# Kernel tuning notes

Hardware: AMD Instinct MI355X
Metric: run time of the kernel (lower is better)

Reference implementation:

```python
import jax, jax.numpy as jnp
import numpy as np

B, TQ, TK, D, H = 2, 2048, 2048, 1024, 16


def setup_inputs() -> dict:
    key = jax.random.key(0)
    ks = jax.random.split(key, 8)
    s = 1.0 / np.sqrt(D)
    x_q = jax.random.normal(ks[0], (B, TQ, D), jnp.float32)
    x_k = jax.random.normal(ks[1], (B, TK, D), jnp.float32)
    x_v = jax.random.normal(ks[2], (B, TK, D), jnp.float32)
    # causal mask, True = masked (matches masked_fill semantics)
    causal = jnp.triu(jnp.ones((TQ, TK), jnp.bool_), k=1)
    attn_mask = jnp.broadcast_to(causal, (B, TQ, TK))
    Wq = jax.random.normal(ks[3], (D, D), jnp.float32) * s
    Wk = jax.random.normal(ks[4], (D, D), jnp.float32) * s
    Wv = jax.random.normal(ks[5], (D, D), jnp.float32) * s
    Wo = jax.random.normal(ks[6], (D, D), jnp.float32) * s
    z = jnp.zeros((D,), jnp.float32)
    return {"x_q": x_q, "x_k": x_k, "x_v": x_v, "attn_mask": attn_mask,
            "Wq": Wq, "bq": z, "Wk": Wk, "bk": z, "Wv": Wv, "bv": z,
            "Wo": Wo, "bo": z, "n_heads": H}


def reference(x_q, x_k, x_v, attn_mask, Wq, bq, Wk, bk, Wv, bv, Wo, bo, n_heads):
    Bv, Tq, Dm = x_q.shape
    Tk = x_k.shape[1]
    dh = Dm // n_heads
    # nn.Linear: y = x @ W^T + b; split heads -> [B, H, T, dh]
    Q = (jnp.einsum('btd,od->bto', x_q, Wq) + bq).reshape(Bv, Tq, n_heads, dh).transpose(0, 2, 1, 3)
    K = (jnp.einsum('btd,od->bto', x_k, Wk) + bk).reshape(Bv, Tk, n_heads, dh).transpose(0, 2, 1, 3)
    V = (jnp.einsum('btd,od->bto', x_v, Wv) + bv).reshape(Bv, Tk, n_heads, dh).transpose(0, 2, 1, 3)
    scale = 1.0 / np.sqrt(dh).astype(np.float32)
    scores = jnp.einsum('bhqd,bhkd->bhqk', Q, K) * scale  # [B,H,Tq,Tk]
    scores = jnp.where(attn_mask[:, None, :, :], -jnp.inf, scores)
    A = jax.nn.softmax(scores, axis=-1)  # dropout p=0.0 -> identity
    out = jnp.einsum('bhqk,bhkd->bhqd', A, V)
    out = out.transpose(0, 2, 1, 3).reshape(Bv, Tq, Dm)
    return jnp.einsum('btd,od->bto', out, Wo) + bo
```

## Files before the change

### kernel.cpp

```cpp
#include <hip/hip_runtime.h>


typedef __attribute__((ext_vector_type(8))) __bf16 bf16x8;
typedef __attribute__((ext_vector_type(4))) float f32x4;
typedef unsigned short u16;

constexpr int BATCH  = 2;
constexpr int TSEQ   = 2048;
constexpr int DMODEL = 1024;
constexpr int NHEAD  = 16;
constexpr int DHEAD  = 64;
constexpr int MROWS  = BATCH * TSEQ;

static __device__ __forceinline__ u16 f2bf(float f) {
  union { float f; unsigned int u; } v; v.f = f;
  unsigned int u = v.u;
  return (u16)((u + 0x7fffu + ((u >> 16) & 1u)) >> 16);
}

static __device__ __forceinline__ void gload16(const void* g, void* l) {
  __builtin_amdgcn_global_load_lds(
      (const __attribute__((address_space(1))) void*)g,
      (__attribute__((address_space(3))) void*)l, 16, 0, 0);
}

__global__ __launch_bounds__(256) void cvt_multi(const float* __restrict__ s0,
                                                 const float* __restrict__ s1,
                                                 const float* __restrict__ s2,
                                                 const float* __restrict__ s3,
                                                 u16* __restrict__ d0, u16* __restrict__ d1,
                                                 u16* __restrict__ d2, u16* __restrict__ d3,
                                                 int n4) {
  const float* s; u16* d;
  switch (blockIdx.y) {
    case 0: s = s0; d = d0; break;
    case 1: s = s1; d = d1; break;
    case 2: s = s2; d = d2; break;
    default: s = s3; d = d3; break;
  }
  int i = blockIdx.x * 256 + threadIdx.x;
  if (i >= n4) return;
  float4 f = ((const float4*)s)[i];
  ushort4 o;
  o.x = f2bf(f.x); o.y = f2bf(f.y); o.z = f2bf(f.z); o.w = f2bf(f.w);
  ((ushort4*)d)[i] = o;
}

template <typename Epi>
static __device__ __forceinline__ void gemm_body(const u16* __restrict__ X_,
                                                 const u16* __restrict__ W_,
                                                 const float* __restrict__ bias,
                                                 Epi epi) {
  __shared__ __align__(16) u16 As[2][4096];
  __shared__ __align__(16) u16 Bs[2][4096];
  const int lane = threadIdx.x & 63, wave = threadIdx.x >> 6;
  const int l16 = lane & 15, lk = lane >> 4;
  const int wm = wave >> 2, wn = wave & 3;
  const int row0 = blockIdx.x * 128, col0 = blockIdx.y * 128;
  constexpr int K = DMODEL;
  const u16* ga = X_ + (size_t)(row0 + wave * 16 + l16) * K + lk * 8;
  const u16* gb = W_ + (size_t)(col0 + wave * 16 + l16) * K + lk * 8;
  f32x4 acc[4][2];
#pragma unroll
  for (int mt = 0; mt < 4; ++mt)
#pragma unroll
    for (int nt = 0; nt < 2; ++nt) acc[mt][nt] = (f32x4){0.f, 0.f, 0.f, 0.f};
  gload16(ga, &As[0][wave * 512]);
  gload16(gb, &Bs[0][wave * 512]);
  __syncthreads();
  int buf = 0;
  for (int ks = 0; ks < K / 32; ++ks) {
    if (ks + 1 < K / 32) {
      gload16(ga + (ks + 1) * 32, &As[buf ^ 1][wave * 512]);
      gload16(gb + (ks + 1) * 32, &Bs[buf ^ 1][wave * 512]);
    }
    bf16x8 a[4], b[2];
#pragma unroll
    for (int mt = 0; mt < 4; ++mt)
      a[mt] = *(const bf16x8*)&As[buf][(wm * 4 + mt) * 512 + lane * 8];
#pragma unroll
    for (int nt = 0; nt < 2; ++nt)
      b[nt] = *(const bf16x8*)&Bs[buf][(wn * 2 + nt) * 512 + lane * 8];
#pragma unroll
    for (int mt = 0; mt < 4; ++mt)
#pragma unroll
      for (int nt = 0; nt < 2; ++nt)
        acc[mt][nt] =
            __builtin_amdgcn_mfma_f32_16x16x32_bf16(a[mt], b[nt], acc[mt][nt], 0, 0, 0);
    __syncthreads();
    buf ^= 1;
  }
#pragma unroll
  for (int mt = 0; mt < 4; ++mt)
#pragma unroll
    for (int nt = 0; nt < 2; ++nt)
#pragma unroll
      for (int r = 0; r < 4; ++r) {
        int m = row0 + wm * 64 + mt * 16 + lk * 4 + r;
        int n = col0 + wn * 32 + nt * 16 + l16;
        float v = acc[mt][nt][r] + bias[n];
        epi(m, n, v);
      }
}

__global__ __launch_bounds__(512) void gemm_qkv(
    const u16* __restrict__ xq, const u16* __restrict__ xk, const u16* __restrict__ xv,
    const u16* __restrict__ wq, const u16* __restrict__ wk, const u16* __restrict__ wv,
    const float* __restrict__ bq, const float* __restrict__ bk, const float* __restrict__ bv,
    u16* __restrict__ Qh, u16* __restrict__ Kh, u16* __restrict__ Vt) {
  const int z = blockIdx.z;
  const u16* X = z == 0 ? xq : (z == 1 ? xk : xv);
  const u16* W = z == 0 ? wq : (z == 1 ? wk : wv);
  const float* bias = z == 0 ? bq : (z == 1 ? bk : bv);
  u16* O01 = z == 0 ? Qh : Kh;
  gemm_body(X, W, bias, [&](int m, int n, float v) {
    int bb = m >> 11, t = m & (TSEQ - 1);
    int h = n >> 6, dd = n & (DHEAD - 1);
    if (z == 0) v *= 0.125f;
    if (z == 2)
      Vt[(((size_t)(bb * NHEAD + h)) * DHEAD + dd) * TSEQ + t] = f2bf(v);
    else
      O01[(((size_t)(bb * NHEAD + h)) * TSEQ + t) * DHEAD + dd] = f2bf(v);
  });
}

__global__ __launch_bounds__(512) void gemm_o(const u16* __restrict__ AO,
                                              const u16* __restrict__ wo,
                                              const float* __restrict__ bias,
                                              float* __restrict__ out) {
  gemm_body(AO, wo, bias,
            [&](int m, int n, float v) { out[(size_t)m * DMODEL + n] = v; });
}

__global__ __launch_bounds__(512, 6) void flash_attn(const u16* __restrict__ Qh,
                                                     const u16* __restrict__ Kh,
                                                     const u16* __restrict__ Vt,
                                                     u16* __restrict__ AO) {
  const int lane = threadIdx.x & 63, wave = threadIdx.x >> 6;
  const int l16 = lane & 15, lk = lane >> 4;
  const int bh = blockIdx.x;
  const int qt = (gridDim.y - 1) - blockIdx.y;
  const int q0 = qt * 128;
  const int b = bh >> 4, h = bh & 15;

  __shared__ __align__(16) u16 Kl[2][4096];
  __shared__ __align__(16) u16 Vl[2][4096];
  __shared__ __align__(16) u16 plds[8][16][72];

  const u16* Qb = Qh + (size_t)bh * TSEQ * DHEAD;
  const u16* Kb = Kh + (size_t)bh * TSEQ * DHEAD;
  const u16* Vb = Vt + (size_t)bh * DHEAD * TSEQ;

  bf16x8 qf[2];
  {
    const u16* qp = Qb + (size_t)(q0 + wave * 16 + l16) * DHEAD + lk * 8;
    qf[0] = *(const bf16x8*)(qp);
    qf[1] = *(const bf16x8*)(qp + 32);
  }

  float mrow[4], lsum[4];
  f32x4 acco[4];
#pragma unroll
  for (int r = 0; r < 4; ++r) { mrow[r] = -1e30f; lsum[r] = 0.f; }
#pragma unroll
  for (int dt = 0; dt < 4; ++dt) acco[dt] = (f32x4){0.f, 0.f, 0.f, 0.f};

  auto stage_kv = [&](int bufi, int kbase) {
    int trow = (wave >> 1) * 16 + l16;
    int dhs = (wave & 1) * 4 + lk;
    gload16(Kb + (size_t)(kbase + trow) * DHEAD + dhs * 8, &Kl[bufi][wave * 512]);
    gload16(Vb + (size_t)trow * TSEQ + kbase + dhs * 8, &Vl[bufi][wave * 512]);
  };

  const int nkb = 2 * qt + 2;
  const int kbdiag = 2 * qt + (wave >> 2);
  stage_kv(0, 0);
  __syncthreads();
  int buf = 0;
  const int qrow_base = q0 + wave * 16 + 4 * lk;

  for (int kb = 0; kb < nkb; ++kb) {
    const int kbase = kb * 64;
    if (kb + 1 < nkb) stage_kv(buf ^ 1, kbase + 64);

    if (kb <= kbdiag) {
      f32x4 s[4];
#pragma unroll
      for (int nt = 0; nt < 4; ++nt) {
        bf16x8 k0f = *(const bf16x8*)&Kl[buf][nt * 1024 + lane * 8];
        bf16x8 k1f = *(const bf16x8*)&Kl[buf][nt * 1024 + 512 + lane * 8];
        f32x4 z = (f32x4){0.f, 0.f, 0.f, 0.f};
        z = __builtin_amdgcn_mfma_f32_16x16x32_bf16(qf[0], k0f, z, 0, 0, 0);
        z = __builtin_amdgcn_mfma_f32_16x16x32_bf16(qf[1], k1f, z, 0, 0, 0);
        s[nt] = z;
      }
      if (kb == kbdiag) {
#pragma unroll
        for (int nt = 0; nt < 4; ++nt)
#pragma unroll
          for (int r = 0; r < 4; ++r) {
            int kcol = kbase + nt * 16 + l16;
            s[nt][r] = (kcol <= qrow_base + r) ? s[nt][r] : -1e30f;
          }
      }
      float pmax[4];
      bool need = false;
#pragma unroll
      for (int r = 0; r < 4; ++r) {
        pmax[r] = fmaxf(fmaxf(s[0][r], s[1][r]), fmaxf(s[2][r], s[3][r]));
        need |= (pmax[r] > mrow[r] + 8.f);
      }
      if (__any(need)) {
#pragma unroll
        for (int r = 0; r < 4; ++r) {
          float mx = pmax[r];
#pragma unroll
          for (int off = 1; off < 16; off <<= 1) mx = fmaxf(mx, __shfl_xor(mx, off, 16));
          float mnew = fmaxf(mrow[r], mx);
          float alpha = __expf(mrow[r] - mnew);
          lsum[r] *= alpha;
#pragma unroll
          for (int dt = 0; dt < 4; ++dt) acco[dt][r] *= alpha;
          mrow[r] = mnew;
        }
      }
#pragma unroll
      for (int r = 0; r < 4; ++r)
#pragma unroll
        for (int nt = 0; nt < 4; ++nt) {
          float p = __expf(s[nt][r] - mrow[r]);
          s[nt][r] = p;
          lsum[r] += p;
        }
#pragma unroll
      for (int nt = 0; nt < 4; ++nt)
#pragma unroll
        for (int r = 0; r < 4; ++r)
          plds[wave][4 * lk + r][nt * 16 + l16] = f2bf(s[nt][r]);
      bf16x8 pf0 = *(const bf16x8*)&plds[wave][l16][lk * 8];
      bf16x8 pf1 = *(const bf16x8*)&plds[wave][l16][32 + lk * 8];
#pragma unroll
      for (int dt = 0; dt < 4; ++dt) {
        bf16x8 v0 = *(const bf16x8*)&Vl[buf][dt * 1024 + lane * 8];
        bf16x8 v1 = *(const bf16x8*)&Vl[buf][dt * 1024 + 512 + lane * 8];
        acco[dt] = __builtin_amdgcn_mfma_f32_16x16x32_bf16(pf0, v0, acco[dt], 0, 0, 0);
        acco[dt] = __builtin_amdgcn_mfma_f32_16x16x32_bf16(pf1, v1, acco[dt], 0, 0, 0);
      }
    }
    __syncthreads();
    buf ^= 1;
  }

#pragma unroll
  for (int r = 0; r < 4; ++r) {
    float t = lsum[r];
#pragma unroll
    for (int off = 1; off < 16; off <<= 1) t += __shfl_xor(t, off, 16);
    lsum[r] = 1.f / t;
  }
#pragma unroll
  for (int dt = 0; dt < 4; ++dt)
#pragma unroll
    for (int r = 0; r < 4; ++r) {
      int t = qrow_base + r;
      int col = h * DHEAD + dt * 16 + l16;
      AO[((size_t)(b * TSEQ + t)) * DMODEL + col] = f2bf(acco[dt][r] * lsum[r]);
    }
}

extern "C" void kernel_launch(void* const* d_in, const int* in_sizes, int n_in,
                              void* d_out, int out_size, void* d_ws, size_t ws_size,
                              hipStream_t stream) {
  const float* x_q = (const float*)d_in[0];
  const float* x_k = (const float*)d_in[1];
  const float* x_v = (const float*)d_in[2];
  const float* Wq = (const float*)d_in[4];
  const float* bq = (const float*)d_in[5];
  const float* Wk = (const float*)d_in[6];
  const float* bk = (const float*)d_in[7];
  const float* Wv = (const float*)d_in[8];
  const float* bv = (const float*)d_in[9];
  const float* Wo = (const float*)d_in[10];
  const float* bo = (const float*)d_in[11];

  const size_t nx = (size_t)MROWS * DMODEL;
  const size_t nw = (size_t)DMODEL * DMODEL;
  u16* ws   = (u16*)d_ws;
  u16* xq_b = ws;
  u16* xk_b = xq_b + nx;
  u16* xv_b = xk_b + nx;
  u16* wq_b = xv_b + nx;
  u16* wk_b = wq_b + nw;
  u16* wv_b = wk_b + nw;
  u16* wo_b = wv_b + nw;
  u16* Qh   = wo_b + nw;
  u16* Kh   = Qh + nx;
  u16* Vt   = Kh + nx;
  u16* AO   = Vt + nx;

  const int n4x = (int)(nx / 4), n4w = (int)(nw / 4);
  cvt_multi<<<dim3((n4x + 255) / 256, 3), 256, 0, stream>>>(
      x_q, x_k, x_v, nullptr, xq_b, xk_b, xv_b, nullptr, n4x);
  cvt_multi<<<dim3((n4w + 255) / 256, 4), 256, 0, stream>>>(
      Wq, Wk, Wv, Wo, wq_b, wk_b, wv_b, wo_b, n4w);

  gemm_qkv<<<dim3(MROWS / 128, DMODEL / 128, 3), 512, 0, stream>>>(
      xq_b, xk_b, xv_b, wq_b, wk_b, wv_b, bq, bk, bv, Qh, Kh, Vt);

  flash_attn<<<dim3(BATCH * NHEAD, TSEQ / 128), 512, 0, stream>>>(Qh, Kh, Vt, AO);

  gemm_o<<<dim3(MROWS / 128, DMODEL / 128), 512, 0, stream>>>(AO, wo_b, bo, (float*)d_out);
}
```

Before: 158.2 us.

## Retile projection GEMMs to 256-thread blocks and narrower output-GEMM tiles

The shared GEMM body is templated on the N tile width and now uses 4 waves of 256 threads instead of 8. Each wave computes a larger 64xBN/2 sub-tile and issues several LDS-staging loads per k-step. The output projection switches to 128x64 tiles, doubling its grid to 512 blocks so more CUs are filled. The intent is more MFMA work per wave and better occupancy (launch bounds 256,4), at the cost of more accumulator registers per thread and fewer waves to hide load latency.

```diff
diff --git a/kernel.cpp b/kernel.cpp
--- a/kernel.cpp
+++ b/kernel.cpp
@@ -46,45 +46,58 @@
   ((ushort4*)d)[i] = o;
 }
 
-template <typename Epi>
+template <int BN, typename Epi>
 static __device__ __forceinline__ void gemm_body(const u16* __restrict__ X_,
                                                  const u16* __restrict__ W_,
                                                  const float* __restrict__ bias,
                                                  Epi epi) {
-  __shared__ __align__(16) u16 As[2][4096];
-  __shared__ __align__(16) u16 Bs[2][4096];
+  constexpr int K = DMODEL;
+  constexpr int NT = BN / 32;
+  __shared__ __align__(16) u16 As[2][8 * 512];
+  __shared__ __align__(16) u16 Bs[2][(BN / 16) * 512];
   const int lane = threadIdx.x & 63, wave = threadIdx.x >> 6;
   const int l16 = lane & 15, lk = lane >> 4;
-  const int wm = wave >> 2, wn = wave & 3;
-  const int row0 = blockIdx.x * 128, col0 = blockIdx.y * 128;
-  constexpr int K = DMODEL;
-  const u16* ga = X_ + (size_t)(row0 + wave * 16 + l16) * K + lk * 8;
-  const u16* gb = W_ + (size_t)(col0 + wave * 16 + l16) * K + lk * 8;
-  f32x4 acc[4][2];
+  const int wm = wave >> 1, wn = wave & 1;
+  const int row0 = blockIdx.x * 128, col0 = blockIdx.y * BN;
+
+  const u16* ga = X_ + (size_t)(row0 + l16) * K + lk * 8;
+  const u16* gb = W_ + (size_t)(col0 + l16) * K + lk * 8;
+
+  f32x4 acc[4][NT];
 #pragma unroll
   for (int mt = 0; mt < 4; ++mt)
 #pragma unroll
-    for (int nt = 0; nt < 2; ++nt) acc[mt][nt] = (f32x4){0.f, 0.f, 0.f, 0.f};
-  gload16(ga, &As[0][wave * 512]);
-  gload16(gb, &Bs[0][wave * 512]);
+    for (int nt = 0; nt < NT; ++nt) acc[mt][nt] = (f32x4){0.f, 0.f, 0.f, 0.f};
+
+  auto stage = [&](int bufi, int ks) {
+#pragma unroll
+    for (int j = 0; j < 2; ++j) {
+      int s = j * 4 + wave;
+      gload16(ga + (size_t)s * 16 * K + ks * 32, &As[bufi][s * 512]);
+    }
+#pragma unroll
+    for (int j = 0; j < BN / 64; ++j) {
+      int s = j * 4 + wave;
+      gload16(gb + (size_t)s * 16 * K + ks * 32, &Bs[bufi][s * 512]);
+    }
+  };
+
+  stage(0, 0);
   __syncthreads();
   int buf = 0;
   for (int ks = 0; ks < K / 32; ++ks) {
-    if (ks + 1 < K / 32) {
-      gload16(ga + (ks + 1) * 32, &As[buf ^ 1][wave * 512]);
-      gload16(gb + (ks + 1) * 32, &Bs[buf ^ 1][wave * 512]);
-    }
-    bf16x8 a[4], b[2];
+    if (ks + 1 < K / 32) stage(buf ^ 1, ks + 1);
+    bf16x8 a[4], b[NT];
 #pragma unroll
     for (int mt = 0; mt < 4; ++mt)
       a[mt] = *(const bf16x8*)&As[buf][(wm * 4 + mt) * 512 + lane * 8];
 #pragma unroll
-    for (int nt = 0; nt < 2; ++nt)
-      b[nt] = *(const bf16x8*)&Bs[buf][(wn * 2 + nt) * 512 + lane * 8];
+    for (int nt = 0; nt < NT; ++nt)
+      b[nt] = *(const bf16x8*)&Bs[buf][(wn * NT + nt) * 512 + lane * 8];
 #pragma unroll
     for (int mt = 0; mt < 4; ++mt)
 #pragma unroll
-      for (int nt = 0; nt < 2; ++nt)
+      for (int nt = 0; nt < NT; ++nt)
         acc[mt][nt] =
             __builtin_amdgcn_mfma_f32_16x16x32_bf16(a[mt], b[nt], acc[mt][nt], 0, 0, 0);
     __syncthreads();
@@ -93,17 +106,17 @@
 #pragma unroll
   for (int mt = 0; mt < 4; ++mt)
 #pragma unroll
-    for (int nt = 0; nt < 2; ++nt)
+    for (int nt = 0; nt < NT; ++nt)
 #pragma unroll
       for (int r = 0; r < 4; ++r) {
         int m = row0 + wm * 64 + mt * 16 + lk * 4 + r;
-        int n = col0 + wn * 32 + nt * 16 + l16;
+        int n = col0 + wn * (BN / 2) + nt * 16 + l16;
         float v = acc[mt][nt][r] + bias[n];
         epi(m, n, v);
       }
 }
 
-__global__ __launch_bounds__(512) void gemm_qkv(
+__global__ __launch_bounds__(256, 4) void gemm_qkv(
     const u16* __restrict__ xq, const u16* __restrict__ xk, const u16* __restrict__ xv,
     const u16* __restrict__ wq, const u16* __restrict__ wk, const u16* __restrict__ wv,
     const float* __restrict__ bq, const float* __restrict__ bk, const float* __restrict__ bv,
@@ -113,7 +126,7 @@
   const u16* W = z == 0 ? wq : (z == 1 ? wk : wv);
   const float* bias = z == 0 ? bq : (z == 1 ? bk : bv);
   u16* O01 = z == 0 ? Qh : Kh;
-  gemm_body(X, W, bias, [&](int m, int n, float v) {
+  gemm_body<128>(X, W, bias, [&](int m, int n, float v) {
     int bb = m >> 11, t = m & (TSEQ - 1);
     int h = n >> 6, dd = n & (DHEAD - 1);
     if (z == 0) v *= 0.125f;
@@ -124,12 +137,12 @@
   });
 }
 
-__global__ __launch_bounds__(512) void gemm_o(const u16* __restrict__ AO,
-                                              const u16* __restrict__ wo,
-                                              const float* __restrict__ bias,
-                                              float* __restrict__ out) {
-  gemm_body(AO, wo, bias,
-            [&](int m, int n, float v) { out[(size_t)m * DMODEL + n] = v; });
+__global__ __launch_bounds__(256, 4) void gemm_o(const u16* __restrict__ AO,
+                                                 const u16* __restrict__ wo,
+                                                 const float* __restrict__ bias,
+                                                 float* __restrict__ out) {
+  gemm_body<64>(AO, wo, bias,
+                [&](int m, int n, float v) { out[(size_t)m * DMODEL + n] = v; });
 }
 
 __global__ __launch_bounds__(512, 6) void flash_attn(const u16* __restrict__ Qh,
@@ -304,10 +317,10 @@
   cvt_multi<<<dim3((n4w + 255) / 256, 4), 256, 0, stream>>>(
       Wq, Wk, Wv, Wo, wq_b, wk_b, wv_b, wo_b, n4w);
 
-  gemm_qkv<<<dim3(MROWS / 128, DMODEL / 128, 3), 512, 0, stream>>>(
+  gemm_qkv<<<dim3(MROWS / 128, DMODEL / 128, 3), 256, 0, stream>>>(
       xq_b, xk_b, xv_b, wq_b, wk_b, wv_b, bq, bk, bv, Qh, Kh, Vt);
 
   flash_attn<<<dim3(BATCH * NHEAD, TSEQ / 128), 512, 0, stream>>>(Qh, Kh, Vt, AO);
 
-  gemm_o<<<dim3(MROWS / 128, DMODEL / 128), 512, 0, stream>>>(AO, wo_b, bo, (float*)d_out);
-}
+  gemm_o<<<dim3(MROWS / 128, DMODEL / 64), 256, 0, stream>>>(AO, wo_b, bo, (float*)d_out);
+}
```

Measured after the change: 160.8 us. About the same (+1.6%).

## Deepen GEMM global-to-LDS pipeline to four buffers with explicit vmcnt waits

Applied to the files above, without the earlier changes.

Replaces the double-buffered K loop in the shared GEMM body with a four-stage ring that keeps three tiles in flight. Explicit s_waitcnt vmcnt counts and a single s_barrier per iteration replace the two __syncthreads calls, and MFMA issue is wrapped in raised wave priority. Launch bounds hint four blocks per CU. The aim is to hide global load latency in the QKV and output projections, at the cost of doubling GEMM LDS use, which may limit occupancy. It also relies on hand-counted vmcnt values being correct for buffer reuse safety.

```diff
diff --git a/kernel.cpp b/kernel.cpp
--- a/kernel.cpp
+++ b/kernel.cpp
@@ -51,29 +51,42 @@
                                                  const u16* __restrict__ W_,
                                                  const float* __restrict__ bias,
                                                  Epi epi) {
-  __shared__ __align__(16) u16 As[2][4096];
-  __shared__ __align__(16) u16 Bs[2][4096];
+  constexpr int K = DMODEL;
+  constexpr int NK = K / 32;
+  __shared__ __align__(16) u16 As[4][4096];
+  __shared__ __align__(16) u16 Bs[4][4096];
   const int lane = threadIdx.x & 63, wave = threadIdx.x >> 6;
   const int l16 = lane & 15, lk = lane >> 4;
   const int wm = wave >> 2, wn = wave & 3;
   const int row0 = blockIdx.x * 128, col0 = blockIdx.y * 128;
-  constexpr int K = DMODEL;
+
   const u16* ga = X_ + (size_t)(row0 + wave * 16 + l16) * K + lk * 8;
   const u16* gb = W_ + (size_t)(col0 + wave * 16 + l16) * K + lk * 8;
+
   f32x4 acc[4][2];
 #pragma unroll
   for (int mt = 0; mt < 4; ++mt)
 #pragma unroll
     for (int nt = 0; nt < 2; ++nt) acc[mt][nt] = (f32x4){0.f, 0.f, 0.f, 0.f};
-  gload16(ga, &As[0][wave * 512]);
-  gload16(gb, &Bs[0][wave * 512]);
-  __syncthreads();
-  int buf = 0;
-  for (int ks = 0; ks < K / 32; ++ks) {
-    if (ks + 1 < K / 32) {
-      gload16(ga + (ks + 1) * 32, &As[buf ^ 1][wave * 512]);
-      gload16(gb + (ks + 1) * 32, &Bs[buf ^ 1][wave * 512]);
-    }
+
+  auto stage = [&](int bufi, int ks) {
+    gload16(ga + ks * 32, &As[bufi][wave * 512]);
+    gload16(gb + ks * 32, &Bs[bufi][wave * 512]);
+  };
+
+  stage(0, 0);
+  stage(1, 1);
+  stage(2, 2);
+
+  for (int ks = 0; ks < NK; ++ks) {
+    const int buf = ks & 3;
+    if (ks < NK - 2)       asm volatile("s_waitcnt vmcnt(4)" ::: "memory");
+    else if (ks == NK - 2) asm volatile("s_waitcnt vmcnt(2)" ::: "memory");
+    else                   asm volatile("s_waitcnt vmcnt(0)" ::: "memory");
+    __builtin_amdgcn_s_barrier();
+    __builtin_amdgcn_sched_barrier(0);
+    if (ks + 3 < NK) stage((ks + 3) & 3, ks + 3);
+
     bf16x8 a[4], b[2];
 #pragma unroll
     for (int mt = 0; mt < 4; ++mt)
@@ -81,15 +94,16 @@
 #pragma unroll
     for (int nt = 0; nt < 2; ++nt)
       b[nt] = *(const bf16x8*)&Bs[buf][(wn * 2 + nt) * 512 + lane * 8];
+    __builtin_amdgcn_s_setprio(1);
 #pragma unroll
     for (int mt = 0; mt < 4; ++mt)
 #pragma unroll
       for (int nt = 0; nt < 2; ++nt)
         acc[mt][nt] =
             __builtin_amdgcn_mfma_f32_16x16x32_bf16(a[mt], b[nt], acc[mt][nt], 0, 0, 0);
-    __syncthreads();
-    buf ^= 1;
-  }
+    __builtin_amdgcn_s_setprio(0);
+  }
+
 #pragma unroll
   for (int mt = 0; mt < 4; ++mt)
 #pragma unroll
@@ -103,7 +117,7 @@
       }
 }
 
-__global__ __launch_bounds__(512) void gemm_qkv(
+__global__ __launch_bounds__(512, 4) void gemm_qkv(
     const u16* __restrict__ xq, const u16* __restrict__ xk, const u16* __restrict__ xv,
     const u16* __restrict__ wq, const u16* __restrict__ wk, const u16* __restrict__ wv,
     const float* __restrict__ bq, const float* __restrict__ bk, const float* __restrict__ bv,
@@ -124,10 +138,10 @@
   });
 }
 
-__global__ __launch_bounds__(512) void gemm_o(const u16* __restrict__ AO,
-                                              const u16* __restrict__ wo,
-                                              const float* __restrict__ bias,
-                                              float* __restrict__ out) {
+__global__ __launch_bounds__(512, 4) void gemm_o(const u16* __restrict__ AO,
+                                                 const u16* __restrict__ wo,
+                                                 const float* __restrict__ bias,
+                                                 float* __restrict__ out) {
   gemm_body(AO, wo, bias,
             [&](int m, int n, float v) { out[(size_t)m * DMODEL + n] = v; });
 }
```

Result: slower. 172.1 us (+8.8%).
